# Kernel tuning notes

Measured on AMD Instinct MI355X. Metric: run time of the kernel, lower is better.

The kernel has to match this reference:

```python
import jax, jax.numpy as jnp
import numpy as np

N = 100000
NNZ = 3200000
K = 3

def setup_inputs() -> dict:
    key = jax.random.key(0)
    ks = jax.random.split(key, 9)
    return {
        "x": jax.random.normal(ks[0], (N, 128), dtype=jnp.float32),
        "vals": jax.random.uniform(ks[1], (NNZ,), dtype=jnp.float32) * (1.0 / 32.0),
        "W1": jax.random.normal(ks[2], (128 * K, 256), dtype=jnp.float32) * 0.05,
        "b1": jax.random.normal(ks[3], (256,), dtype=jnp.float32) * 0.05,
        "W2": jax.random.normal(ks[4], (256 * K, 64), dtype=jnp.float32) * 0.05,
        "b2": jax.random.normal(ks[5], (64,), dtype=jnp.float32) * 0.05,
        "rows": jax.random.randint(ks[6], (NNZ,), 0, N, dtype=jnp.int32),
        "cols": jax.random.randint(ks[7], (NNZ,), 0, N, dtype=jnp.int32),
        "idx": jax.random.randint(ks[8], (50000,), 0, N, dtype=jnp.int32),
    }

def _spmm(rows, cols, vals, x):
    # sparse [N,N] @ dense [N,F] via gather + segment_sum
    return jax.ops.segment_sum(vals[:, None] * x[cols], rows, num_segments=N)

def _cheb_basis(x, rows, cols, vals, k):
    # Chebyshev recurrence: T0=x, T1=L x, T_m = 2 L T_{m-1} - T_{m-2}
    xs = [x]
    if k > 1:
        x0, x1 = x, _spmm(rows, cols, vals, x)
        xs.append(x1)
        for _ in range(2, k):
            x2 = 2.0 * _spmm(rows, cols, vals, x1) - x0
            xs.append(x2)
            x0, x1 = x1, x2
    # match torch layout: [N, F, K] -> [N, F*K] (per-feature K contiguous)
    return jnp.stack(xs, axis=2).reshape(x.shape[0], -1)

def reference(x, vals, W1, b1, W2, b2, rows, cols, idx):
    h = _cheb_basis(x, rows, cols, vals, K) @ W1 + b1
    h = jax.nn.relu(h)  # dropout omitted (eval mode)
    out = _cheb_basis(h, rows, cols, vals, K) @ W2 + b2
    return out[idx]
```

## Files before the change

### kernel.cpp

```cpp
#include <hip/hip_runtime.h>
#include <hip/hip_bf16.h>

typedef __attribute__((ext_vector_type(8))) __bf16 bf16x8;
typedef __attribute__((ext_vector_type(4))) float floatx4;
typedef unsigned short ushort_t;
typedef unsigned int uint_t;

#define N_NODES 100000
#define NNZ_E   3200000
#define N_IDX   50000
#define NB_BKT  196
#define PTILE   8192
#define PBLOCKS 391

__device__ __forceinline__ float bf2f(uint_t u16) {
  union { float f; uint_t i; } v; v.i = u16 << 16; return v.f;
}
__device__ __forceinline__ unsigned short f2bf(float f) {
  union { float f; uint_t i; } v; v.f = f;
  uint_t x = v.i;
  return (unsigned short)((x + 0x7FFFu + ((x >> 16) & 1u)) >> 16);
}


__global__ __launch_bounds__(256) void k_bhist(const int* __restrict__ rows,
                                               int* __restrict__ bcnt) {
  __shared__ int h[NB_BKT];
  for (int i = threadIdx.x; i < NB_BKT; i += 256) h[i] = 0;
  __syncthreads();
  int base = blockIdx.x * PTILE;
  for (int i = threadIdx.x; i < PTILE; i += 256) {
    int e = base + i;
    if (e < NNZ_E) atomicAdd(&h[rows[e] >> 9], 1);
  }
  __syncthreads();
  for (int i = threadIdx.x; i < NB_BKT; i += 256)
    if (h[i]) atomicAdd(&bcnt[i], h[i]);
}

__global__ void k_bscan(const int* __restrict__ bcnt, int* __restrict__ bbase,
                        int* __restrict__ bcur) {
  __shared__ int ts[256];
  int t = threadIdx.x;
  int v = (t < NB_BKT) ? bcnt[t] : 0;
  ts[t] = v;
  __syncthreads();
  for (int off = 1; off < 256; off <<= 1) {
    int x = ts[t];
    int a = (t >= off) ? ts[t - off] : 0;
    __syncthreads();
    ts[t] = x + a;
    __syncthreads();
  }
  if (t < NB_BKT) {
    int b = (t == 0) ? 0 : ts[t - 1];
    bbase[t] = b;
    bcur[t] = b;
  }
}

__global__ __launch_bounds__(256) void k_part(const int* __restrict__ rows,
                                              const int* __restrict__ cols,
                                              const float* __restrict__ vals,
                                              int* __restrict__ bcur,
                                              int2* __restrict__ tmp) {
  __shared__ int h[NB_BKT];
  for (int i = threadIdx.x; i < NB_BKT; i += 256) h[i] = 0;
  __syncthreads();
  int base = blockIdx.x * PTILE;
  for (int i = threadIdx.x; i < PTILE; i += 256) {
    int e = base + i;
    if (e < NNZ_E) atomicAdd(&h[rows[e] >> 9], 1);
  }
  __syncthreads();
  for (int i = threadIdx.x; i < NB_BKT; i += 256) {
    int c = h[i];
    h[i] = c ? atomicAdd(&bcur[i], c) : 0;
  }
  __syncthreads();
  for (int i = threadIdx.x; i < PTILE; i += 256) {
    int e = base + i;
    if (e < NNZ_E) {
      int rr = rows[e];
      int p = atomicAdd(&h[rr >> 9], 1);
      int2 o;
      o.x = cols[e] | ((rr & 511) << 17);
      o.y = __float_as_int(vals[e]);
      tmp[p] = o;
    }
  }
}

__global__ __launch_bounds__(512) void k_sort(const int* __restrict__ bbase,
                                              const int2* __restrict__ tmp,
                                              int2* __restrict__ edges,
                                              int* __restrict__ rowptr) {
  __shared__ int cnt[512];
  __shared__ int ts[512];
  int b = blockIdx.x, t = threadIdx.x;
  int s = bbase[b];
  int epos = (b == NB_BKT - 1) ? NNZ_E : bbase[b + 1];
  cnt[t] = 0;
  __syncthreads();
  for (int i = s + t; i < epos; i += 512)
    atomicAdd(&cnt[(tmp[i].x >> 17) & 511], 1);
  __syncthreads();
  ts[t] = cnt[t];
  __syncthreads();
  for (int off = 1; off < 512; off <<= 1) {
    int x = ts[t];
    int a = (t >= off) ? ts[t - off] : 0;
    __syncthreads();
    ts[t] = x + a;
    __syncthreads();
  }
  int pre = (t == 0) ? 0 : ts[t - 1];
  int grow = b * 512 + t;
  if (grow < N_NODES) rowptr[grow] = s + pre;
  cnt[t] = s + pre;
  __syncthreads();
  for (int i = s + t; i < epos; i += 512) {
    int2 p = tmp[i];
    int rl = (p.x >> 17) & 511;
    int pos = atomicAdd(&cnt[rl], 1);
    int2 o;
    o.x = p.x & 0x1FFFF;
    o.y = p.y;
    edges[pos] = o;
  }
  if (b == 0 && t == 0) rowptr[N_NODES] = NNZ_E;
}


__global__ void k_cvt(const float4* __restrict__ x, ushort4* __restrict__ xb) {
  int i = blockIdx.x * blockDim.x + threadIdx.x;
  if (i < N_NODES * 128 / 4) {
    float4 v = x[i];
    ushort4 o;
    o.x = f2bf(v.x); o.y = f2bf(v.y); o.z = f2bf(v.z); o.w = f2bf(v.w);
    xb[i] = o;
  }
}


__global__ void k_prepW1(const float* __restrict__ W, ushort_t* __restrict__ Wp) {
  int kp = blockIdx.x;
  int n  = threadIdx.x;
  int ch = kp >> 7;
  int f  = kp & 127;
  float v;
  if (ch == 0)      v = W[(f*3+0)*256+n] - W[(f*3+2)*256+n];
  else if (ch == 1) v = W[(f*3+1)*256+n];
  else              v = 2.0f * W[(f*3+2)*256+n];
  int kb = kp >> 5, kr = kp & 31;
  int lane = ((kr >> 3) << 4) | (n & 15);
  Wp[(((size_t)kb * 16 + (n >> 4)) * 64 + lane) * 8 + (kr & 7)] = f2bf(v);
}

__global__ void k_prepW2(const float* __restrict__ W, ushort_t* __restrict__ Wp) {
  int f = blockIdx.x;
  int c = threadIdx.x;
  int g = c >> 6, n = c & 63;
  float v;
  if (g == 0)      v = W[(f*3+0)*64+n] - W[(f*3+2)*64+n];
  else if (g == 1) v = W[(f*3+1)*64+n];
  else             v = 2.0f * W[(f*3+2)*64+n];
  int kb = f >> 5, kr = f & 31;
  int nb = c >> 4;
  int lane = ((kr >> 3) << 4) | (c & 15);
  Wp[(((size_t)kb * 12 + nb) * 64 + lane) * 8 + (kr & 7)] = f2bf(v);
}


__global__ __launch_bounds__(256) void k_spmm128(
    const int* __restrict__ rowptr, const int2* __restrict__ edges,
    const ushort_t* __restrict__ in, ushort_t* __restrict__ out) {
  int r = __builtin_amdgcn_readfirstlane(blockIdx.x * 4 + (threadIdx.x >> 6));
  int f = threadIdx.x & 63;
  int e0 = rowptr[r], e1 = rowptr[r + 1];
  float a0 = 0.f, a1 = 0.f;
  int e = e0;
  for (; e + 16 <= e1; e += 16) {
    int2 E[16];
#pragma unroll
    for (int j = 0; j < 16; ++j) E[j] = edges[e + j];
    uint_t q[16];
#pragma unroll
    for (int j = 0; j < 16; ++j)
      q[j] = *(const uint_t*)(in + (size_t)E[j].x * 128 + 2 * f);
#pragma unroll
    for (int j = 0; j < 16; ++j) {
      float v = __int_as_float(E[j].y);
      a0 = fmaf(v, bf2f(q[j] & 0xFFFFu), a0);
      a1 = fmaf(v, bf2f(q[j] >> 16), a1);
    }
  }
  for (; e + 4 <= e1; e += 4) {
    int2 E[4];
#pragma unroll
    for (int j = 0; j < 4; ++j) E[j] = edges[e + j];
    uint_t q[4];
#pragma unroll
    for (int j = 0; j < 4; ++j)
      q[j] = *(const uint_t*)(in + (size_t)E[j].x * 128 + 2 * f);
#pragma unroll
    for (int j = 0; j < 4; ++j) {
      float v = __int_as_float(E[j].y);
      a0 = fmaf(v, bf2f(q[j] & 0xFFFFu), a0);
      a1 = fmaf(v, bf2f(q[j] >> 16), a1);
    }
  }
  for (; e < e1; ++e) {
    int2 E = edges[e];
    uint_t q = *(const uint_t*)(in + (size_t)E.x * 128 + 2 * f);
    float v = __int_as_float(E.y);
    a0 = fmaf(v, bf2f(q & 0xFFFFu), a0);
    a1 = fmaf(v, bf2f(q >> 16), a1);
  }
  uint_t o = ((uint_t)f2bf(a1) << 16) | (uint_t)f2bf(a0);
  *(uint_t*)(out + (size_t)r * 128 + 2 * f) = o;
}


__global__ __launch_bounds__(256) void k_spmm64_add(
    const int* __restrict__ rowptr, const int2* __restrict__ edges,
    const ushort_t* __restrict__ p2, const ushort_t* __restrict__ p1,
    ushort_t* __restrict__ u) {
  int r = __builtin_amdgcn_readfirstlane(blockIdx.x * 4 + (threadIdx.x >> 6));
  int f = threadIdx.x & 63;
  int e0 = rowptr[r], e1 = rowptr[r + 1];
  float a = 0.f;
  int e = e0;
  for (; e + 16 <= e1; e += 16) {
    int2 E[16];
#pragma unroll
    for (int j = 0; j < 16; ++j) E[j] = edges[e + j];
    ushort_t q[16];
#pragma unroll
    for (int j = 0; j < 16; ++j) q[j] = p2[(size_t)E[j].x * 64 + f];
#pragma unroll
    for (int j = 0; j < 16; ++j)
      a = fmaf(__int_as_float(E[j].y), bf2f(q[j]), a);
  }
  for (; e + 4 <= e1; e += 4) {
    int2 E[4];
#pragma unroll
    for (int j = 0; j < 4; ++j) E[j] = edges[e + j];
    ushort_t q[4];
#pragma unroll
    for (int j = 0; j < 4; ++j) q[j] = p2[(size_t)E[j].x * 64 + f];
#pragma unroll
    for (int j = 0; j < 4; ++j)
      a = fmaf(__int_as_float(E[j].y), bf2f(q[j]), a);
  }
  for (; e < e1; ++e) {
    int2 E = edges[e];
    a = fmaf(__int_as_float(E.y), bf2f(p2[(size_t)E.x * 64 + f]), a);
  }
  float b = a + bf2f(p1[(size_t)r * 64 + f]);
  u[(size_t)r * 64 + f] = f2bf(b);
}


__global__ __launch_bounds__(256) void k_spmm64_idx(
    const int* __restrict__ rowptr, const int2* __restrict__ edges,
    const ushort_t* __restrict__ u, const float* __restrict__ p0,
    const int* __restrict__ idx, float* __restrict__ out) {
  int o = __builtin_amdgcn_readfirstlane(blockIdx.x * 4 + (threadIdx.x >> 6));
  int f = threadIdx.x & 63;
  int r = __builtin_amdgcn_readfirstlane(idx[o]);
  int e0 = rowptr[r], e1 = rowptr[r + 1];
  float a = 0.f;
  int e = e0;
  for (; e + 16 <= e1; e += 16) {
    int2 E[16];
#pragma unroll
    for (int j = 0; j < 16; ++j) E[j] = edges[e + j];
    ushort_t q[16];
#pragma unroll
    for (int j = 0; j < 16; ++j) q[j] = u[(size_t)E[j].x * 64 + f];
#pragma unroll
    for (int j = 0; j < 16; ++j)
      a = fmaf(__int_as_float(E[j].y), bf2f(q[j]), a);
  }
  for (; e + 4 <= e1; e += 4) {
    int2 E[4];
#pragma unroll
    for (int j = 0; j < 4; ++j) E[j] = edges[e + j];
    ushort_t q[4];
#pragma unroll
    for (int j = 0; j < 4; ++j) q[j] = u[(size_t)E[j].x * 64 + f];
#pragma unroll
    for (int j = 0; j < 4; ++j)
      a = fmaf(__int_as_float(E[j].y), bf2f(q[j]), a);
  }
  for (; e < e1; ++e) {
    int2 E = edges[e];
    a = fmaf(__int_as_float(E.y), bf2f(u[(size_t)E.x * 64 + f]), a);
  }
  float res = p0[(size_t)r * 64 + f] + a;
  out[(size_t)o * 64 + f] = res;
}


__global__ __launch_bounds__(256) void k_gemm1(
    const ushort_t* __restrict__ A0, const ushort_t* __restrict__ A1,
    const ushort_t* __restrict__ A2, const ushort_t* __restrict__ Bp,
    const float* __restrict__ bias, ushort_t* __restrict__ h) {
  int wid = (blockIdx.x * 256 + threadIdx.x) >> 6;
  int lane = threadIdx.x & 63;
  int mt = wid >> 1, ng = wid & 1;
  int mr = mt * 16 + (lane & 15);
  int ko = (lane >> 4) << 3;
  floatx4 acc[8] = {};
#pragma unroll
  for (int c = 0; c < 3; ++c) {
    const ushort_t* Ab = (c == 0 ? A0 : c == 1 ? A1 : A2) + (size_t)mr * 128 + ko;
#pragma unroll
    for (int kb = 0; kb < 4; ++kb) {
      bf16x8 a = *(const bf16x8*)(Ab + kb * 32);
      int kbg = c * 4 + kb;
      const ushort_t* Bb = Bp + (((size_t)(kbg * 16 + ng * 8)) * 64 + lane) * 8;
#pragma unroll
      for (int nt = 0; nt < 8; ++nt) {
        bf16x8 b = *(const bf16x8*)(Bb + (size_t)nt * 64 * 8);
        acc[nt] = __builtin_amdgcn_mfma_f32_16x16x32_bf16(a, b, acc[nt], 0, 0, 0);
      }
    }
  }
  int col0 = ng * 128 + (lane & 15);
  int r0 = mt * 16 + ((lane >> 4) << 2);
#pragma unroll
  for (int nt = 0; nt < 8; ++nt) {
    int col = col0 + nt * 16;
    float bv = bias[col];
#pragma unroll
    for (int rg = 0; rg < 4; ++rg) {
      float v = acc[nt][rg] + bv;
      v = v > 0.f ? v : 0.f;
      h[(size_t)(r0 + rg) * 256 + col] = f2bf(v);
    }
  }
}


__global__ __launch_bounds__(256) void k_gemm2(
    const ushort_t* __restrict__ A, const ushort_t* __restrict__ Bp,
    const float* __restrict__ bias, float* __restrict__ p0,
    ushort_t* __restrict__ p1, ushort_t* __restrict__ p2) {
  int wid = (blockIdx.x * 256 + threadIdx.x) >> 6;
  if (wid >= 18750) return;
  int lane = threadIdx.x & 63;
  int mt = wid / 3, ng = wid - mt * 3;
  int mr = mt * 16 + (lane & 15);
  int ko = (lane >> 4) << 3;
  floatx4 acc[4] = {};
  const ushort_t* Ab = A + (size_t)mr * 256 + ko;
#pragma unroll
  for (int kb = 0; kb < 8; ++kb) {
    bf16x8 a = *(const bf16x8*)(Ab + kb * 32);
    const ushort_t* Bb = Bp + (((size_t)(kb * 12 + ng * 4)) * 64 + lane) * 8;
#pragma unroll
    for (int nt = 0; nt < 4; ++nt) {
      bf16x8 b = *(const bf16x8*)(Bb + (size_t)nt * 64 * 8);
      acc[nt] = __builtin_amdgcn_mfma_f32_16x16x32_bf16(a, b, acc[nt], 0, 0, 0);
    }
  }
  int c16 = lane & 15;
  int r0 = mt * 16 + ((lane >> 4) << 2);
  if (ng == 0) {
#pragma unroll
    for (int nt = 0; nt < 4; ++nt) {
      float bv = bias[nt * 16 + c16];
#pragma unroll
      for (int rg = 0; rg < 4; ++rg)
        p0[(size_t)(r0 + rg) * 64 + nt * 16 + c16] = acc[nt][rg] + bv;
    }
  } else {
    ushort_t* dst = (ng == 1) ? p1 : p2;
#pragma unroll
    for (int nt = 0; nt < 4; ++nt)
#pragma unroll
      for (int rg = 0; rg < 4; ++rg)
        dst[(size_t)(r0 + rg) * 64 + nt * 16 + c16] = f2bf(acc[nt][rg]);
  }
}


extern "C" void kernel_launch(void* const* d_in, const int* in_sizes, int n_in,
                              void* d_out, int out_size, void* d_ws, size_t ws_size,
                              hipStream_t stream) {
  const float* x    = (const float*)d_in[0];
  const float* vals = (const float*)d_in[1];
  const float* W1   = (const float*)d_in[2];
  const float* b1   = (const float*)d_in[3];
  const float* W2   = (const float*)d_in[4];
  const float* b2   = (const float*)d_in[5];
  const int*   rows = (const int*)d_in[6];
  const int*   cols = (const int*)d_in[7];
  const int*   idx  = (const int*)d_in[8];
  float* out = (float*)d_out;

  char* w = (char*)d_ws;
  size_t off = 0;
  auto take = [&](size_t b) -> char* {
    char* p = w + off;
    off += (b + 255) & ~(size_t)255;
    return p;
  };
  int*      bcnt    = (int*)take((size_t)NB_BKT * 4);
  int*      bbase   = (int*)take((size_t)NB_BKT * 4);
  int*      bcur    = (int*)take((size_t)NB_BKT * 4);
  int*      rowptr  = (int*)take((size_t)(N_NODES + 1) * 4);
  int2*     tmp     = (int2*)take((size_t)NNZ_E * 8);
  int2*     edges   = (int2*)take((size_t)NNZ_E * 8);
  ushort_t* xb      = (ushort_t*)take((size_t)N_NODES * 128 * 2);
  ushort_t* T1a     = (ushort_t*)take((size_t)N_NODES * 128 * 2);
  ushort_t* U1      = (ushort_t*)take((size_t)N_NODES * 128 * 2);
  ushort_t* h       = (ushort_t*)take((size_t)N_NODES * 256 * 2);
  ushort_t* W1p     = (ushort_t*)take((size_t)384 * 256 * 2);
  ushort_t* W2p     = (ushort_t*)take((size_t)256 * 192 * 2);

  float*    p0 = (float*)xb;
  ushort_t* p1 = T1a;
  ushort_t* p2 = T1a + (size_t)N_NODES * 64;
  ushort_t* u  = U1;

  hipMemsetAsync(bcnt, 0, (size_t)NB_BKT * 4, stream);
  k_bhist<<<PBLOCKS, 256, 0, stream>>>(rows, bcnt);
  k_bscan<<<1, 256, 0, stream>>>(bcnt, bbase, bcur);
  k_part<<<PBLOCKS, 256, 0, stream>>>(rows, cols, vals, bcur, tmp);
  k_sort<<<NB_BKT, 512, 0, stream>>>(bbase, tmp, edges, rowptr);

  k_cvt<<<(N_NODES * 128 / 4 + 255) / 256, 256, 0, stream>>>((const float4*)x, (ushort4*)xb);
  k_prepW1<<<384, 256, 0, stream>>>(W1, W1p);
  k_prepW2<<<256, 192, 0, stream>>>(W2, W2p);

  k_spmm128<<<N_NODES / 4, 256, 0, stream>>>(rowptr, edges, xb, T1a);
  k_spmm128<<<N_NODES / 4, 256, 0, stream>>>(rowptr, edges, T1a, U1);
  k_gemm1<<<3125, 256, 0, stream>>>(xb, T1a, U1, W1p, b1, h);

  k_gemm2<<<4688, 256, 0, stream>>>(h, W2p, b2, p0, p1, p2);
  k_spmm64_add<<<N_NODES / 4, 256, 0, stream>>>(rowptr, edges, p2, p1, u);
  k_spmm64_idx<<<N_IDX / 4, 256, 0, stream>>>(rowptr, edges, u, p0, idx, out);
}
```

Measured before the change: 667.4 us.

## Split SpMM wave lanes across edges with wide vector gathers and LDS-staged edges

```diff
diff --git a/kernel.cpp b/kernel.cpp
--- a/kernel.cpp
+++ b/kernel.cpp
@@ -20,6 +20,9 @@
   union { float f; uint_t i; } v; v.f = f;
   uint_t x = v.i;
   return (unsigned short)((x + 0x7FFFu + ((x >> 16) & 1u)) >> 16);
+}
+__device__ __forceinline__ uint_t pk(float lo, float hi) {
+  return ((uint_t)f2bf(hi) << 16) | (uint_t)f2bf(lo);
 }
 
 
@@ -175,50 +178,64 @@
 __global__ __launch_bounds__(256) void k_spmm128(
     const int* __restrict__ rowptr, const int2* __restrict__ edges,
     const ushort_t* __restrict__ in, ushort_t* __restrict__ out) {
-  int r = __builtin_amdgcn_readfirstlane(blockIdx.x * 4 + (threadIdx.x >> 6));
-  int f = threadIdx.x & 63;
+  __shared__ int2 eb[4][32];
+  int w = threadIdx.x >> 6, lane = threadIdx.x & 63;
+  int l4 = lane & 15, bg = lane >> 4;
+  int r = __builtin_amdgcn_readfirstlane(blockIdx.x * 4 + w);
   int e0 = rowptr[r], e1 = rowptr[r + 1];
-  float a0 = 0.f, a1 = 0.f;
-  int e = e0;
-  for (; e + 16 <= e1; e += 16) {
-    int2 E[16];
-#pragma unroll
-    for (int j = 0; j < 16; ++j) E[j] = edges[e + j];
-    uint_t q[16];
-#pragma unroll
-    for (int j = 0; j < 16; ++j)
-      q[j] = *(const uint_t*)(in + (size_t)E[j].x * 128 + 2 * f);
-#pragma unroll
-    for (int j = 0; j < 16; ++j) {
-      float v = __int_as_float(E[j].y);
-      a0 = fmaf(v, bf2f(q[j] & 0xFFFFu), a0);
-      a1 = fmaf(v, bf2f(q[j] >> 16), a1);
-    }
-  }
-  for (; e + 4 <= e1; e += 4) {
-    int2 E[4];
-#pragma unroll
-    for (int j = 0; j < 4; ++j) E[j] = edges[e + j];
-    uint_t q[4];
-#pragma unroll
-    for (int j = 0; j < 4; ++j)
-      q[j] = *(const uint_t*)(in + (size_t)E[j].x * 128 + 2 * f);
-#pragma unroll
-    for (int j = 0; j < 4; ++j) {
-      float v = __int_as_float(E[j].y);
-      a0 = fmaf(v, bf2f(q[j] & 0xFFFFu), a0);
-      a1 = fmaf(v, bf2f(q[j] >> 16), a1);
-    }
-  }
-  for (; e < e1; ++e) {
-    int2 E = edges[e];
-    uint_t q = *(const uint_t*)(in + (size_t)E.x * 128 + 2 * f);
-    float v = __int_as_float(E.y);
-    a0 = fmaf(v, bf2f(q & 0xFFFFu), a0);
-    a1 = fmaf(v, bf2f(q >> 16), a1);
-  }
-  uint_t o = ((uint_t)f2bf(a1) << 16) | (uint_t)f2bf(a0);
-  *(uint_t*)(out + (size_t)r * 128 + 2 * f) = o;
+  if (lane < 32) eb[w][lane] = make_int2(0, 0);
+  const ushort_t* inb = in + 8 * l4;
+  float a0=0.f,a1=0.f,a2=0.f,a3=0.f,a4=0.f,a5=0.f,a6=0.f,a7=0.f;
+  for (int e = e0; e < e1; e += 32) {
+    int rem = e1 - e; if (rem > 32) rem = 32;
+    if (lane < rem) eb[w][lane] = edges[e + lane];
+    int pmax = (rem + 7) >> 3;
+    int2 cA = eb[w][bg];
+    int2 cB = eb[w][4 + bg];
+    uint4 qA = *(const uint4*)(inb + (size_t)cA.x * 128);
+    uint4 qB = *(const uint4*)(inb + (size_t)cB.x * 128);
+    for (int p = 1; p < pmax; ++p) {
+      int2 nA = eb[w][8 * p + bg];
+      int2 nB = eb[w][8 * p + 4 + bg];
+      uint4 mA = *(const uint4*)(inb + (size_t)nA.x * 128);
+      uint4 mB = *(const uint4*)(inb + (size_t)nB.x * 128);
+      float vA = __int_as_float(cA.y);
+      float vB = __int_as_float(cB.y);
+      a0 = fmaf(vA, bf2f(qA.x & 0xFFFFu), a0); a1 = fmaf(vA, bf2f(qA.x >> 16), a1);
+      a2 = fmaf(vA, bf2f(qA.y & 0xFFFFu), a2); a3 = fmaf(vA, bf2f(qA.y >> 16), a3);
+      a4 = fmaf(vA, bf2f(qA.z & 0xFFFFu), a4); a5 = fmaf(vA, bf2f(qA.z >> 16), a5);
+      a6 = fmaf(vA, bf2f(qA.w & 0xFFFFu), a6); a7 = fmaf(vA, bf2f(qA.w >> 16), a7);
+      a0 = fmaf(vB, bf2f(qB.x & 0xFFFFu), a0); a1 = fmaf(vB, bf2f(qB.x >> 16), a1);
+      a2 = fmaf(vB, bf2f(qB.y & 0xFFFFu), a2); a3 = fmaf(vB, bf2f(qB.y >> 16), a3);
+      a4 = fmaf(vB, bf2f(qB.z & 0xFFFFu), a4); a5 = fmaf(vB, bf2f(qB.z >> 16), a5);
+      a6 = fmaf(vB, bf2f(qB.w & 0xFFFFu), a6); a7 = fmaf(vB, bf2f(qB.w >> 16), a7);
+      cA = nA; cB = nB; qA = mA; qB = mB;
+    }
+    int ebase = 8 * (pmax - 1);
+    float vA = (ebase + bg < rem) ? __int_as_float(cA.y) : 0.f;
+    float vB = (ebase + 4 + bg < rem) ? __int_as_float(cB.y) : 0.f;
+    a0 = fmaf(vA, bf2f(qA.x & 0xFFFFu), a0); a1 = fmaf(vA, bf2f(qA.x >> 16), a1);
+    a2 = fmaf(vA, bf2f(qA.y & 0xFFFFu), a2); a3 = fmaf(vA, bf2f(qA.y >> 16), a3);
+    a4 = fmaf(vA, bf2f(qA.z & 0xFFFFu), a4); a5 = fmaf(vA, bf2f(qA.z >> 16), a5);
+    a6 = fmaf(vA, bf2f(qA.w & 0xFFFFu), a6); a7 = fmaf(vA, bf2f(qA.w >> 16), a7);
+    a0 = fmaf(vB, bf2f(qB.x & 0xFFFFu), a0); a1 = fmaf(vB, bf2f(qB.x >> 16), a1);
+    a2 = fmaf(vB, bf2f(qB.y & 0xFFFFu), a2); a3 = fmaf(vB, bf2f(qB.y >> 16), a3);
+    a4 = fmaf(vB, bf2f(qB.z & 0xFFFFu), a4); a5 = fmaf(vB, bf2f(qB.z >> 16), a5);
+    a6 = fmaf(vB, bf2f(qB.w & 0xFFFFu), a6); a7 = fmaf(vB, bf2f(qB.w >> 16), a7);
+  }
+  a0 += __shfl_xor(a0, 16); a0 += __shfl_xor(a0, 32);
+  a1 += __shfl_xor(a1, 16); a1 += __shfl_xor(a1, 32);
+  a2 += __shfl_xor(a2, 16); a2 += __shfl_xor(a2, 32);
+  a3 += __shfl_xor(a3, 16); a3 += __shfl_xor(a3, 32);
+  a4 += __shfl_xor(a4, 16); a4 += __shfl_xor(a4, 32);
+  a5 += __shfl_xor(a5, 16); a5 += __shfl_xor(a5, 32);
+  a6 += __shfl_xor(a6, 16); a6 += __shfl_xor(a6, 32);
+  a7 += __shfl_xor(a7, 16); a7 += __shfl_xor(a7, 32);
+  if (bg == 0) {
+    uint4 o;
+    o.x = pk(a0, a1); o.y = pk(a2, a3); o.z = pk(a4, a5); o.w = pk(a6, a7);
+    *(uint4*)(out + (size_t)r * 128 + 8 * l4) = o;
+  }
 }
 
 
@@ -226,39 +243,57 @@
     const int* __restrict__ rowptr, const int2* __restrict__ edges,
     const ushort_t* __restrict__ p2, const ushort_t* __restrict__ p1,
     ushort_t* __restrict__ u) {
-  int r = __builtin_amdgcn_readfirstlane(blockIdx.x * 4 + (threadIdx.x >> 6));
-  int f = threadIdx.x & 63;
+  __shared__ int2 eb[4][32];
+  int w = threadIdx.x >> 6, lane = threadIdx.x & 63;
+  int l4 = lane & 15, bg = lane >> 4;
+  int r = __builtin_amdgcn_readfirstlane(blockIdx.x * 4 + w);
   int e0 = rowptr[r], e1 = rowptr[r + 1];
-  float a = 0.f;
-  int e = e0;
-  for (; e + 16 <= e1; e += 16) {
-    int2 E[16];
-#pragma unroll
-    for (int j = 0; j < 16; ++j) E[j] = edges[e + j];
-    ushort_t q[16];
-#pragma unroll
-    for (int j = 0; j < 16; ++j) q[j] = p2[(size_t)E[j].x * 64 + f];
-#pragma unroll
-    for (int j = 0; j < 16; ++j)
-      a = fmaf(__int_as_float(E[j].y), bf2f(q[j]), a);
-  }
-  for (; e + 4 <= e1; e += 4) {
-    int2 E[4];
-#pragma unroll
-    for (int j = 0; j < 4; ++j) E[j] = edges[e + j];
-    ushort_t q[4];
-#pragma unroll
-    for (int j = 0; j < 4; ++j) q[j] = p2[(size_t)E[j].x * 64 + f];
-#pragma unroll
-    for (int j = 0; j < 4; ++j)
-      a = fmaf(__int_as_float(E[j].y), bf2f(q[j]), a);
-  }
-  for (; e < e1; ++e) {
-    int2 E = edges[e];
-    a = fmaf(__int_as_float(E.y), bf2f(p2[(size_t)E.x * 64 + f]), a);
-  }
-  float b = a + bf2f(p1[(size_t)r * 64 + f]);
-  u[(size_t)r * 64 + f] = f2bf(b);
+  if (lane < 32) eb[w][lane] = make_int2(0, 0);
+  const ushort_t* inb = p2 + 4 * l4;
+  float a0=0.f,a1=0.f,a2=0.f,a3=0.f;
+  for (int e = e0; e < e1; e += 32) {
+    int rem = e1 - e; if (rem > 32) rem = 32;
+    if (lane < rem) eb[w][lane] = edges[e + lane];
+    int pmax = (rem + 7) >> 3;
+    int2 cA = eb[w][bg];
+    int2 cB = eb[w][4 + bg];
+    uint2 qA = *(const uint2*)(inb + (size_t)cA.x * 64);
+    uint2 qB = *(const uint2*)(inb + (size_t)cB.x * 64);
+    for (int p = 1; p < pmax; ++p) {
+      int2 nA = eb[w][8 * p + bg];
+      int2 nB = eb[w][8 * p + 4 + bg];
+      uint2 mA = *(const uint2*)(inb + (size_t)nA.x * 64);
+      uint2 mB = *(const uint2*)(inb + (size_t)nB.x * 64);
+      float vA = __int_as_float(cA.y);
+      float vB = __int_as_float(cB.y);
+      a0 = fmaf(vA, bf2f(qA.x & 0xFFFFu), a0); a1 = fmaf(vA, bf2f(qA.x >> 16), a1);
+      a2 = fmaf(vA, bf2f(qA.y & 0xFFFFu), a2); a3 = fmaf(vA, bf2f(qA.y >> 16), a3);
+      a0 = fmaf(vB, bf2f(qB.x & 0xFFFFu), a0); a1 = fmaf(vB, bf2f(qB.x >> 16), a1);
+      a2 = fmaf(vB, bf2f(qB.y & 0xFFFFu), a2); a3 = fmaf(vB, bf2f(qB.y >> 16), a3);
+      cA = nA; cB = nB; qA = mA; qB = mB;
+    }
+    int ebase = 8 * (pmax - 1);
+    float vA = (ebase + bg < rem) ? __int_as_float(cA.y) : 0.f;
+    float vB = (ebase + 4 + bg < rem) ? __int_as_float(cB.y) : 0.f;
+    a0 = fmaf(vA, bf2f(qA.x & 0xFFFFu), a0); a1 = fmaf(vA, bf2f(qA.x >> 16), a1);
+    a2 = fmaf(vA, bf2f(qA.y & 0xFFFFu), a2); a3 = fmaf(vA, bf2f(qA.y >> 16), a3);
+    a0 = fmaf(vB, bf2f(qB.x & 0xFFFFu), a0); a1 = fmaf(vB, bf2f(qB.x >> 16), a1);
+    a2 = fmaf(vB, bf2f(qB.y & 0xFFFFu), a2); a3 = fmaf(vB, bf2f(qB.y >> 16), a3);
+  }
+  a0 += __shfl_xor(a0, 16); a0 += __shfl_xor(a0, 32);
+  a1 += __shfl_xor(a1, 16); a1 += __shfl_xor(a1, 32);
+  a2 += __shfl_xor(a2, 16); a2 += __shfl_xor(a2, 32);
+  a3 += __shfl_xor(a3, 16); a3 += __shfl_xor(a3, 32);
+  if (bg == 0) {
+    uint2 pp = *(const uint2*)(p1 + (size_t)r * 64 + 4 * l4);
+    float b0 = a0 + bf2f(pp.x & 0xFFFFu);
+    float b1 = a1 + bf2f(pp.x >> 16);
+    float b2 = a2 + bf2f(pp.y & 0xFFFFu);
+    float b3 = a3 + bf2f(pp.y >> 16);
+    uint2 o;
+    o.x = pk(b0, b1); o.y = pk(b2, b3);
+    *(uint2*)(u + (size_t)r * 64 + 4 * l4) = o;
+  }
 }
 
 
@@ -266,40 +301,54 @@
     const int* __restrict__ rowptr, const int2* __restrict__ edges,
     const ushort_t* __restrict__ u, const float* __restrict__ p0,
     const int* __restrict__ idx, float* __restrict__ out) {
-  int o = __builtin_amdgcn_readfirstlane(blockIdx.x * 4 + (threadIdx.x >> 6));
-  int f = threadIdx.x & 63;
+  __shared__ int2 eb[4][32];
+  int w = threadIdx.x >> 6, lane = threadIdx.x & 63;
+  int l4 = lane & 15, bg = lane >> 4;
+  int o = __builtin_amdgcn_readfirstlane(blockIdx.x * 4 + w);
   int r = __builtin_amdgcn_readfirstlane(idx[o]);
   int e0 = rowptr[r], e1 = rowptr[r + 1];
-  float a = 0.f;
-  int e = e0;
-  for (; e + 16 <= e1; e += 16) {
-    int2 E[16];
-#pragma unroll
-    for (int j = 0; j < 16; ++j) E[j] = edges[e + j];
-    ushort_t q[16];
-#pragma unroll
-    for (int j = 0; j < 16; ++j) q[j] = u[(size_t)E[j].x * 64 + f];
-#pragma unroll
-    for (int j = 0; j < 16; ++j)
-      a = fmaf(__int_as_float(E[j].y), bf2f(q[j]), a);
-  }
-  for (; e + 4 <= e1; e += 4) {
-    int2 E[4];
-#pragma unroll
-    for (int j = 0; j < 4; ++j) E[j] = edges[e + j];
-    ushort_t q[4];
-#pragma unroll
-    for (int j = 0; j < 4; ++j) q[j] = u[(size_t)E[j].x * 64 + f];
-#pragma unroll
-    for (int j = 0; j < 4; ++j)
-      a = fmaf(__int_as_float(E[j].y), bf2f(q[j]), a);
-  }
-  for (; e < e1; ++e) {
-    int2 E = edges[e];
-    a = fmaf(__int_as_float(E.y), bf2f(u[(size_t)E.x * 64 + f]), a);
-  }
-  float res = p0[(size_t)r * 64 + f] + a;
-  out[(size_t)o * 64 + f] = res;
+  if (lane < 32) eb[w][lane] = make_int2(0, 0);
+  const ushort_t* inb = u + 4 * l4;
+  float a0=0.f,a1=0.f,a2=0.f,a3=0.f;
+  for (int e = e0; e < e1; e += 32) {
+    int rem = e1 - e; if (rem > 32) rem = 32;
+    if (lane < rem) eb[w][lane] = edges[e + lane];
+    int pmax = (rem + 7) >> 3;
+    int2 cA = eb[w][bg];
+    int2 cB = eb[w][4 + bg];
+    uint2 qA = *(const uint2*)(inb + (size_t)cA.x * 64);
+    uint2 qB = *(const uint2*)(inb + (size_t)cB.x * 64);
+    for (int p = 1; p < pmax; ++p) {
+      int2 nA = eb[w][8 * p + bg];
+      int2 nB = eb[w][8 * p + 4 + bg];
+      uint2 mA = *(const uint2*)(inb + (size_t)nA.x * 64);
+      uint2 mB = *(const uint2*)(inb + (size_t)nB.x * 64);
+      float vA = __int_as_float(cA.y);
+      float vB = __int_as_float(cB.y);
+      a0 = fmaf(vA, bf2f(qA.x & 0xFFFFu), a0); a1 = fmaf(vA, bf2f(qA.x >> 16), a1);
+      a2 = fmaf(vA, bf2f(qA.y & 0xFFFFu), a2); a3 = fmaf(vA, bf2f(qA.y >> 16), a3);
+      a0 = fmaf(vB, bf2f(qB.x & 0xFFFFu), a0); a1 = fmaf(vB, bf2f(qB.x >> 16), a1);
+      a2 = fmaf(vB, bf2f(qB.y & 0xFFFFu), a2); a3 = fmaf(vB, bf2f(qB.y >> 16), a3);
+      cA = nA; cB = nB; qA = mA; qB = mB;
+    }
+    int ebase = 8 * (pmax - 1);
+    float vA = (ebase + bg < rem) ? __int_as_float(cA.y) : 0.f;
+    float vB = (ebase + 4 + bg < rem) ? __int_as_float(cB.y) : 0.f;
+    a0 = fmaf(vA, bf2f(qA.x & 0xFFFFu), a0); a1 = fmaf(vA, bf2f(qA.x >> 16), a1);
+    a2 = fmaf(vA, bf2f(qA.y & 0xFFFFu), a2); a3 = fmaf(vA, bf2f(qA.y >> 16), a3);
+    a0 = fmaf(vB, bf2f(qB.x & 0xFFFFu), a0); a1 = fmaf(vB, bf2f(qB.x >> 16), a1);
+    a2 = fmaf(vB, bf2f(qB.y & 0xFFFFu), a2); a3 = fmaf(vB, bf2f(qB.y >> 16), a3);
+  }
+  a0 += __shfl_xor(a0, 16); a0 += __shfl_xor(a0, 32);
+  a1 += __shfl_xor(a1, 16); a1 += __shfl_xor(a1, 32);
+  a2 += __shfl_xor(a2, 16); a2 += __shfl_xor(a2, 32);
+  a3 += __shfl_xor(a3, 16); a3 += __shfl_xor(a3, 32);
+  if (bg == 0) {
+    float4 b = *(const float4*)(p0 + (size_t)r * 64 + 4 * l4);
+    float4 ww;
+    ww.x = b.x + a0; ww.y = b.y + a1; ww.z = b.z + a2; ww.w = b.w + a3;
+    *(float4*)(out + (size_t)o * 64 + 4 * l4) = ww;
+  }
 }
 
 
```

Result: no change. 672.6 us (+0.8%).
